# Kernel tuning notes

Measured on AMD Instinct MI355X. Metric: run time of the kernel, lower is better.

Reference implementation:

```python
import jax, jax.numpy as jnp
import numpy as np

D = 256
H = 4
HD = D // H


def rotate_half(x):
    xp = x.reshape(x.shape[:-1] + (-1, 2))
    x1, x2 = xp[..., 0], xp[..., 1]
    return jnp.stack((-x2, x1), axis=-1).reshape(x.shape)


def apply_rope(freqs, t):
    # freqs: [2, B, 1, N, HD]; t: [B, H, N, HD]
    return t * freqs[0] + rotate_half(t) * freqs[1]


def layernorm(x, g, b, eps=1e-5):
    m = jnp.mean(x, axis=-1, keepdims=True)
    v = jnp.var(x, axis=-1, keepdims=True)
    return (x - m) * jax.lax.rsqrt(v + eps) * g + b


def ffn(z, W1, b1, g, be, W2, b2):
    h = layernorm(z @ W1 + b1, g, be)
    h = jax.nn.gelu(h, approximate=False)
    return h @ W2 + b2


def heads_split(t):
    B, N, _ = t.shape
    return t.reshape(B, N, H, HD).transpose(0, 2, 1, 3)  # [B,H,N,HD]


def heads_merge(t):
    B, h, N, hd = t.shape
    return t.transpose(0, 2, 1, 3).reshape(B, N, h * hd)


def sdpa(q, k, v):
    s = q.shape[-1] ** (-0.5)
    sim = jnp.einsum('bhid,bhjd->bhij', q, k) * s
    attn = jax.nn.softmax(sim, axis=-1)
    return jnp.einsum('bhij,bhjd->bhid', attn, v)


def self_block(x, enc, Wqkv, bqkv, Wo, bo, W1, b1, g, be, W2, b2):
    B, N, _ = x.shape
    qkv = (x @ Wqkv + bqkv).reshape(B, N, H, HD, 3).transpose(0, 2, 1, 3, 4)
    q, k, v = qkv[..., 0], qkv[..., 1], qkv[..., 2]
    q = apply_rope(enc, q)
    k = apply_rope(enc, k)
    msg = heads_merge(sdpa(q, k, v)) @ Wo + bo
    return x + ffn(jnp.concatenate([x, msg], axis=-1), W1, b1, g, be, W2, b2)


def cross_block(x0, x1, Wqk, bqk, Wv, bv, Wo, bo, W1, b1, g, be, W2, b2):
    qk0 = heads_split(x0 @ Wqk + bqk)
    qk1 = heads_split(x1 @ Wqk + bqk)
    v0 = heads_split(x0 @ Wv + bv)
    v1 = heads_split(x1 @ Wv + bv)
    s = HD ** (-0.5)
    qk0 = qk0 * (s ** 0.5)
    qk1 = qk1 * (s ** 0.5)
    sim = jnp.einsum('bhid,bhjd->bhij', qk0, qk1)
    attn01 = jax.nn.softmax(sim, axis=-1)
    attn10 = jax.nn.softmax(sim.transpose(0, 1, 3, 2), axis=-1)
    m0 = jnp.einsum('bhij,bhjd->bhid', attn01, v1)
    m1 = jnp.einsum('bhij,bhjd->bhid', attn10, v0)
    m0 = heads_merge(m0) @ Wo + bo
    m1 = heads_merge(m1) @ Wo + bo
    x0 = x0 + ffn(jnp.concatenate([x0, m0], axis=-1), W1, b1, g, be, W2, b2)
    x1 = x1 + ffn(jnp.concatenate([x1, m1], axis=-1), W1, b1, g, be, W2, b2)
    return x0, x1


def setup_inputs() -> dict:
    key = jax.random.key(0)
    ks = jax.random.split(key, 24)
    B, N = 4, 2048
    desc0 = jax.random.normal(ks[0], (B, N, D), jnp.float32)
    desc1 = jax.random.normal(ks[1], (B, N, D), jnp.float32)
    encoding0 = jax.random.uniform(ks[2], (2, B, 1, N, HD), jnp.float32)
    encoding1 = jax.random.uniform(ks[3], (2, B, 1, N, HD), jnp.float32)

    def lin(k, fin, fout):
        k1, k2 = jax.random.split(k)
        W = jax.random.normal(k1, (fin, fout), jnp.float32) * (fin ** -0.5)
        b = jax.random.normal(k2, (fout,), jnp.float32) * 0.01
        return W, b

    Wqkv, bqkv = lin(ks[4], D, 3 * D)
    Wo_s, bo_s = lin(ks[5], D, D)
    W1_s, b1_s = lin(ks[6], 2 * D, 2 * D)
    g_s = jnp.ones((2 * D,), jnp.float32)
    be_s = jnp.zeros((2 * D,), jnp.float32)
    W2_s, b2_s = lin(ks[7], 2 * D, D)
    Wqk_c, bqk_c = lin(ks[8], D, D)
    Wv_c, bv_c = lin(ks[9], D, D)
    Wo_c, bo_c = lin(ks[10], D, D)
    W1_c, b1_c = lin(ks[11], 2 * D, 2 * D)
    g_c = jnp.ones((2 * D,), jnp.float32)
    be_c = jnp.zeros((2 * D,), jnp.float32)
    W2_c, b2_c = lin(ks[12], 2 * D, D)
    return dict(desc0=desc0, desc1=desc1, encoding0=encoding0, encoding1=encoding1,
                Wqkv=Wqkv, bqkv=bqkv, Wo_s=Wo_s, bo_s=bo_s,
                W1_s=W1_s, b1_s=b1_s, g_s=g_s, be_s=be_s, W2_s=W2_s, b2_s=b2_s,
                Wqk_c=Wqk_c, bqk_c=bqk_c, Wv_c=Wv_c, bv_c=bv_c, Wo_c=Wo_c, bo_c=bo_c,
                W1_c=W1_c, b1_c=b1_c, g_c=g_c, be_c=be_c, W2_c=W2_c, b2_c=b2_c)


def reference(desc0, desc1, encoding0, encoding1,
              Wqkv, bqkv, Wo_s, bo_s, W1_s, b1_s, g_s, be_s, W2_s, b2_s,
              Wqk_c, bqk_c, Wv_c, bv_c, Wo_c, bo_c, W1_c, b1_c, g_c, be_c, W2_c, b2_c):
    d0 = self_block(desc0, encoding0, Wqkv, bqkv, Wo_s, bo_s, W1_s, b1_s, g_s, be_s, W2_s, b2_s)
    d1 = self_block(desc1, encoding1, Wqkv, bqkv, Wo_s, bo_s, W1_s, b1_s, g_s, be_s, W2_s, b2_s)
    return cross_block(d0, d1, Wqk_c, bqk_c, Wv_c, bv_c, Wo_c, bo_c, W1_c, b1_c, g_c, be_c, W2_c, b2_c)
```

## Files before the change

kernel.cpp:

```cpp
#include <hip/hip_runtime.h>
#include <math.h>

#define BB 4
#define HH 4
#define NN 2048
#define DD 256
#define HDIM 64
#define NTOK 8192
#define NTOK2 16384

typedef __attribute__((ext_vector_type(8))) __bf16 bf16x8;
typedef __attribute__((ext_vector_type(8))) unsigned short ushort8;
typedef __attribute__((ext_vector_type(4))) float floatx4;
typedef __attribute__((ext_vector_type(4))) short short4v;

union U8 { ushort8 u; bf16x8 b; };
union U4 { unsigned int u[2]; unsigned long long l; short4v s; };

#define MFMA16(a, b, c) __builtin_amdgcn_mfma_f32_16x16x16bf16_1k(a, b, c, 0, 0, 0)

__device__ __forceinline__ unsigned short f2bf(float x) {
    unsigned int u = __float_as_uint(x);
    u += 0x7FFF + ((u >> 16) & 1);
    return (unsigned short)(u >> 16);
}
__device__ __forceinline__ float bf2f(unsigned short u) {
    return __uint_as_float(((unsigned int)u) << 16);
}
__device__ __forceinline__ unsigned int pkbf(float a, float b) {
    return ((__float_as_uint(a) + 0x8000u) >> 16) |
           ((__float_as_uint(b) + 0x8000u) & 0xFFFF0000u);
}

struct WTab {
    const float* w[9];
    unsigned short* o[9];
    int K[9];
    int N[9];
    int t0[10];
};

__global__ __launch_bounds__(256) void wtrans(WTab tab)
{
    __shared__ float lds[32][33];
    const int t = threadIdx.x;
    int bid = blockIdx.x;
    int s = 0;
    while (bid >= tab.t0[s + 1]) s++;
    const int ti = bid - tab.t0[s];
    const int K = tab.K[s], N = tab.N[s];
    const int tx = ti % (N / 32), ty = ti / (N / 32);
    const int k0 = ty * 32, n0 = tx * 32;
    const float* W = tab.w[s];
    unsigned short* Wt = tab.o[s];

    {
        int r = t >> 3, c = (t & 7) * 4;
        float4 a = *(const float4*)&W[(size_t)(k0 + r) * N + n0 + c];
        lds[r][c] = a.x; lds[r][c+1] = a.y; lds[r][c+2] = a.z; lds[r][c+3] = a.w;
    }
    __syncthreads();
    {
        int n = t >> 3, kq = (t & 7) * 4;
        ushort4 p;
        p.x = f2bf(lds[kq+0][n]); p.y = f2bf(lds[kq+1][n]);
        p.z = f2bf(lds[kq+2][n]); p.w = f2bf(lds[kq+3][n]);
        *(ushort4*)&Wt[(size_t)(n0 + n) * K + k0 + kq] = p;
    }
}

__global__ __launch_bounds__(256) void gemm_mfma(
    const unsigned short* __restrict__ A, int lda,
    const unsigned short* __restrict__ Wt, int K,
    const float* __restrict__ bias, const float* __restrict__ bias2, int mode,
    float* outF, unsigned short* outH0, unsigned short* outH1,
    unsigned short* outH2,
    int ldc, const float* R0, const float* R1)
{
    __shared__ __align__(16) unsigned short As[128 * 40];
    __shared__ __align__(16) unsigned short Bs[128 * 40];
    const int t = threadIdx.x;
    const int w = t >> 6, lane = t & 63, quad = lane >> 4, l15 = lane & 15;
    const int m0 = blockIdx.y * 128, n0 = blockIdx.x * 128;
    const int wm = (w >> 1) * 64, wn = (w & 1) * 64;
    const int sr = t >> 1, sc = (t & 1) * 16;

    const unsigned short* Ap = A  + (size_t)(m0 + sr) * lda + sc;
    const unsigned short* Bp = Wt + (size_t)(n0 + sr) * K   + sc;

    ushort8 pa0 = *(const ushort8*)(Ap);
    ushort8 pa1 = *(const ushort8*)(Ap + 8);
    ushort8 pb0 = *(const ushort8*)(Bp);
    ushort8 pb1 = *(const ushort8*)(Bp + 8);

    floatx4 acc[4][4];
    #pragma unroll
    for (int i = 0; i < 4; i++)
        #pragma unroll
        for (int j = 0; j < 4; j++) acc[i][j] = (floatx4){0.f, 0.f, 0.f, 0.f};

    const int nk = K >> 5;
    for (int kk = 0; kk < nk; kk++) {
        *(ushort8*)&As[sr * 40 + sc]     = pa0;
        *(ushort8*)&As[sr * 40 + sc + 8] = pa1;
        *(ushort8*)&Bs[sr * 40 + sc]     = pb0;
        *(ushort8*)&Bs[sr * 40 + sc + 8] = pb1;
        __syncthreads();
        if (kk + 1 < nk) {
            int ko = (kk + 1) * 32;
            pa0 = *(const ushort8*)(Ap + ko);
            pa1 = *(const ushort8*)(Ap + ko + 8);
            pb0 = *(const ushort8*)(Bp + ko);
            pb1 = *(const ushort8*)(Bp + ko + 8);
        }
        U8 af[4], bf[4];
        #pragma unroll
        for (int i = 0; i < 4; i++)
            af[i].u = *(const ushort8*)&As[(wm + i * 16 + l15) * 40 + quad * 8];
        #pragma unroll
        for (int j = 0; j < 4; j++)
            bf[j].u = *(const ushort8*)&Bs[(wn + j * 16 + l15) * 40 + quad * 8];
        #pragma unroll
        for (int i = 0; i < 4; i++)
            #pragma unroll
            for (int j = 0; j < 4; j++)
                acc[i][j] = __builtin_amdgcn_mfma_f32_16x16x32_bf16(af[i].b, bf[j].b, acc[i][j], 0, 0, 0);
        __syncthreads();
    }

    #pragma unroll
    for (int i = 0; i < 4; i++) {
        #pragma unroll
        for (int j = 0; j < 4; j++) {
            int col = n0 + wn + j * 16 + l15;
            float bv = (mode == 2 && col >= 256) ? bias2[col & 255] : bias[col];
            #pragma unroll
            for (int r = 0; r < 4; r++) {
                int grow = m0 + wm + i * 16 + quad * 4 + r;
                float v = acc[i][j][r] + bv;
                if (mode == 1) {
                    outH0[(size_t)grow * ldc + col] = f2bf(v);
                } else if (mode == 2) {
                    int cc = col & 255;
                    int h = cc >> 6, d = cc & 63;
                    int ds = grow >> 13, b = (grow >> 11) & 3, n = grow & 2047;
                    int bh = ds * 16 + b * 4 + h;
                    if (col < 256)
                        outH0[((size_t)bh * NN + n) * HDIM + d] = f2bf(v);
                    else
                        outH1[((size_t)bh * HDIM + d) * NN + n] = f2bf(v);
                } else if (mode == 3) {
                    int sel = col % 3, cc = col / 3;
                    int h = cc >> 6, d = cc & 63;
                    int ds = grow >> 13, b = (grow >> 11) & 3, n = grow & 2047;
                    int bh = ds * 16 + b * 4 + h;
                    if (sel == 0)
                        outH0[((size_t)bh * NN + n) * HDIM + d] = f2bf(v);
                    else if (sel == 1)
                        outH1[((size_t)bh * NN + n) * HDIM + d] = f2bf(v);
                    else
                        outH2[((size_t)bh * HDIM + d) * NN + n] = f2bf(v);
                } else {
                    const float* R = (grow < NTOK) ? R0 : R1;
                    float vv = v + R[(size_t)(grow & 8191) * 256 + col];
                    outF[(size_t)grow * 256 + col] = vv;
                    if (outH0) outH0[(size_t)grow * 256 + col] = f2bf(vv);
                    if (outH1) outH1[(size_t)grow * 512 + col] = f2bf(vv);
                }
            }
        }
    }
}

__global__ __launch_bounds__(256) void rope_k(unsigned short* __restrict__ qb,
                                              unsigned short* __restrict__ kb,
                                              const float* __restrict__ enc0,
                                              const float* __restrict__ enc1)
{
    int i = blockIdx.x * 256 + threadIdx.x;
    int dp = (i & 31) * 2;
    int n  = (i >> 5) & (NN - 1);
    int h  = (i >> 16) & 3;
    int b  = (i >> 18) & 3;
    int ds = (i >> 20) & 1;
    int bf = (i >> 21) & 1;
    unsigned short* tq = (bf ? kb : qb) +
        (((size_t)(ds * 16 + b * 4 + h)) * NN + n) * HDIM + dp;
    const float* e0 = (ds ? enc1 : enc0) + ((size_t)b * NN + n) * HDIM + dp;
    const float* e1 = e0 + (size_t)BB * NN * HDIM;
    float x0 = bf2f(tq[0]), x1 = bf2f(tq[1]);
    float y0 = x0 * e0[0] - x1 * e1[0];
    float y1 = x1 * e0[1] + x0 * e1[1];
    tq[0] = f2bf(y0); tq[1] = f2bf(y1);
}

__global__ __launch_bounds__(256) void flash_attn(
    const unsigned short* __restrict__ Q, const unsigned short* __restrict__ K,
    const unsigned short* __restrict__ V, unsigned short* __restrict__ O,
    int kvx, float qscale)
{
    __shared__ __align__(16) unsigned short Ks[64 * 72];
    __shared__ __align__(16) unsigned short Vt[64 * 72];

    const int t    = threadIdx.x;
    const int w    = t >> 6;
    const int lane = t & 63;
    const int quad = lane >> 4;
    const int l15  = lane & 15;
    const int bh   = blockIdx.y;
    const int kbh  = bh ^ kvx;
    const int q0   = blockIdx.x * 64;

    const unsigned short* Qb  = Q + (size_t)bh  * NN * HDIM;
    const unsigned short* Kb  = K + (size_t)kbh * NN * HDIM;
    const unsigned short* VTb = V + (size_t)kbh * NN * HDIM;

    const int srf = t >> 3, scf = (t & 7) * 8;

    const int qrow = q0 + w * 16 + l15;
    bf16x8 qf0, qf1;
    {
        U8 r0, r1, x0, x1;
        r0.u = *(const ushort8*)&Qb[(size_t)qrow * HDIM + quad * 8];
        r1.u = *(const ushort8*)&Qb[(size_t)qrow * HDIM + 32 + quad * 8];
        #pragma unroll
        for (int j = 0; j < 8; j++) {
            x0.u[j] = f2bf(bf2f(r0.u[j]) * qscale);
            x1.u[j] = f2bf(bf2f(r1.u[j]) * qscale);
        }
        qf0 = x0.b; qf1 = x1.b;
    }

    floatx4 o[4];
    #pragma unroll
    for (int c = 0; c < 4; c++) o[c] = (floatx4){0.f, 0.f, 0.f, 0.f};
    float m = -1e30f, l = 0.f;

    ushort8 ka0 = *(const ushort8*)&Kb[(size_t)srf * HDIM + scf];
    ushort8 ka1 = *(const ushort8*)&Kb[(size_t)(srf + 32) * HDIM + scf];
    ushort8 va0 = *(const ushort8*)&VTb[(size_t)srf * NN + scf];
    ushort8 va1 = *(const ushort8*)&VTb[(size_t)(srf + 32) * NN + scf];

    for (int j0 = 0; j0 < NN; j0 += 64) {
        *(ushort8*)&Ks[srf * 72 + scf]        = ka0;
        *(ushort8*)&Ks[(srf + 32) * 72 + scf] = ka1;
        *(ushort8*)&Vt[srf * 72 + scf]        = va0;
        *(ushort8*)&Vt[(srf + 32) * 72 + scf] = va1;
        __syncthreads();
        if (j0 + 64 < NN) {
            int jn = j0 + 64;
            ka0 = *(const ushort8*)&Kb[(size_t)(jn + srf) * HDIM + scf];
            ka1 = *(const ushort8*)&Kb[(size_t)(jn + srf + 32) * HDIM + scf];
            va0 = *(const ushort8*)&VTb[(size_t)srf * NN + jn + scf];
            va1 = *(const ushort8*)&VTb[(size_t)(srf + 32) * NN + jn + scf];
        }

        floatx4 s[4];
        #pragma unroll
        for (int t4 = 0; t4 < 4; t4++) {
            U8 k0, k1;
            k0.u = *(const ushort8*)&Ks[(t4 * 16 + l15) * 72 + quad * 8];
            k1.u = *(const ushort8*)&Ks[(t4 * 16 + l15) * 72 + 32 + quad * 8];
            floatx4 z = (floatx4){0.f, 0.f, 0.f, 0.f};
            z = __builtin_amdgcn_mfma_f32_16x16x32_bf16(k0.b, qf0, z, 0, 0, 0);
            z = __builtin_amdgcn_mfma_f32_16x16x32_bf16(k1.b, qf1, z, 0, 0, 0);
            s[t4] = z;
        }

        float mx = s[0][0];
        #pragma unroll
        for (int t4 = 0; t4 < 4; t4++)
            #pragma unroll
            for (int r = 0; r < 4; r++) mx = fmaxf(mx, s[t4][r]);
        mx = fmaxf(mx, __shfl_xor(mx, 16, 64));
        mx = fmaxf(mx, __shfl_xor(mx, 32, 64));
        float mn = fmaxf(m, mx);
        float al = exp2f(m - mn);
        m = mn;
        float rs = 0.f;
        #pragma unroll
        for (int t4 = 0; t4 < 4; t4++)
            #pragma unroll
            for (int r = 0; r < 4; r++) {
                float p = exp2f(s[t4][r] - mn);
                s[t4][r] = p;
                rs += p;
            }
        rs += __shfl_xor(rs, 16, 64);
        rs += __shfl_xor(rs, 32, 64);
        l = l * al + rs;
        #pragma unroll
        for (int c = 0; c < 4; c++)
            #pragma unroll
            for (int r = 0; r < 4; r++) o[c][r] *= al;

        short4v pf[4];
        #pragma unroll
        for (int t4 = 0; t4 < 4; t4++) {
            U4 pk;
            pk.u[0] = pkbf(s[t4][0], s[t4][1]);
            pk.u[1] = pkbf(s[t4][2], s[t4][3]);
            pf[t4] = pk.s;
        }

        #pragma unroll
        for (int c = 0; c < 4; c++) {
            #pragma unroll
            for (int t4 = 0; t4 < 4; t4++) {
                U4 vf;
                vf.l = *(const unsigned long long*)
                    &Vt[(c * 16 + l15) * 72 + t4 * 16 + quad * 4];
                o[c] = MFMA16(vf.s, pf[t4], o[c]);
            }
        }
        __syncthreads();
    }

    const int ds = bh >> 4, b = (bh >> 2) & 3, h = bh & 3;
    const int q = q0 + w * 16 + l15;
    const size_t row = (size_t)ds * NTOK + b * NN + q;
    float inv = 1.f / l;
    #pragma unroll
    for (int c = 0; c < 4; c++) {
        ushort4 pk;
        pk.x = f2bf(o[c][0] * inv);
        pk.y = f2bf(o[c][1] * inv);
        pk.z = f2bf(o[c][2] * inv);
        pk.w = f2bf(o[c][3] * inv);
        *(ushort4*)&O[row * DD + h * HDIM + c * 16 + quad * 4] = pk;
    }
}

__global__ __launch_bounds__(256) void ln_gelu(
    unsigned short* __restrict__ hb, const float* __restrict__ g,
    const float* __restrict__ be)
{
    __shared__ float r1[4], r2[4];
    const int t = threadIdx.x;
    const size_t row = blockIdx.x;
    unsigned short* ip = hb + row * 512;
    float x0 = bf2f(ip[t]), x1 = bf2f(ip[t + 256]);
    float s = x0 + x1, ss = x0 * x0 + x1 * x1;
    #pragma unroll
    for (int o = 32; o > 0; o >>= 1) { s += __shfl_down(s, o); ss += __shfl_down(ss, o); }
    if ((t & 63) == 0) { r1[t >> 6] = s; r2[t >> 6] = ss; }
    __syncthreads();
    float S  = r1[0] + r1[1] + r1[2] + r1[3];
    float SS = r2[0] + r2[1] + r2[2] + r2[3];
    float mean = S * (1.f / 512.f);
    float var  = SS * (1.f / 512.f) - mean * mean;
    float inv  = rsqrtf(var + 1e-5f);
    float y0 = (x0 - mean) * inv * g[t]       + be[t];
    float y1 = (x1 - mean) * inv * g[t + 256] + be[t + 256];
    ip[t]       = f2bf(0.5f * y0 * (1.f + erff(y0 * 0.70710678f)));
    ip[t + 256] = f2bf(0.5f * y1 * (1.f + erff(y1 * 0.70710678f)));
}

__global__ __launch_bounds__(256) void copy_to_cat(
    const float* __restrict__ s0, const float* __restrict__ s1,
    unsigned short* __restrict__ cat)
{
    int i = blockIdx.x * 256 + threadIdx.x;
    int row = i >> 6, c4 = (i & 63) * 4;
    const float* s = (row < NTOK) ? s0 : s1;
    float4 a = *(const float4*)&s[(size_t)(row & 8191) * 256 + c4];
    ushort4 p = { f2bf(a.x), f2bf(a.y), f2bf(a.z), f2bf(a.w) };
    *(ushort4*)&cat[(size_t)row * 512 + c4] = p;
}

extern "C" void kernel_launch(void* const* d_in, const int* in_sizes, int n_in,
                              void* d_out, int out_size, void* d_ws, size_t ws_size,
                              hipStream_t stream)
{
    const float* desc0 = (const float*)d_in[0];
    const float* desc1 = (const float*)d_in[1];
    const float* enc0  = (const float*)d_in[2];
    const float* enc1  = (const float*)d_in[3];
    const float* Wqkv  = (const float*)d_in[4];  const float* bqkv  = (const float*)d_in[5];
    const float* Wo_s  = (const float*)d_in[6];  const float* bo_s  = (const float*)d_in[7];
    const float* W1_s  = (const float*)d_in[8];  const float* b1_s  = (const float*)d_in[9];
    const float* g_s   = (const float*)d_in[10]; const float* be_s  = (const float*)d_in[11];
    const float* W2_s  = (const float*)d_in[12]; const float* b2_s  = (const float*)d_in[13];
    const float* Wqk_c = (const float*)d_in[14]; const float* bqk_c = (const float*)d_in[15];
    const float* Wv_c  = (const float*)d_in[16]; const float* bv_c  = (const float*)d_in[17];
    const float* Wo_c  = (const float*)d_in[18]; const float* bo_c  = (const float*)d_in[19];
    const float* W1_c  = (const float*)d_in[20]; const float* b1_c  = (const float*)d_in[21];
    const float* g_c   = (const float*)d_in[22]; const float* be_c  = (const float*)d_in[23];
    const float* W2_c  = (const float*)d_in[24]; const float* b2_c  = (const float*)d_in[25];

    char* ws = (char*)d_ws;
    unsigned short* wt  = (unsigned short*)ws;
    unsigned short* qb  = (unsigned short*)(ws + 2490368);
    unsigned short* kb  = (unsigned short*)(ws + 10878976);
    unsigned short* msg = (unsigned short*)(ws + 19267584);
    unsigned short* vb  = (unsigned short*)(ws + 27656192);
    unsigned short* cat = (unsigned short*)(ws + 36044800);
    unsigned short* hb  = (unsigned short*)(ws + 52822016);
    unsigned short* dbf = (unsigned short*)(ws + 86376448);

    unsigned short* t_qkv = wt;
    unsigned short* t_wos = wt + 196608;
    unsigned short* t_w1s = wt + 262144;
    unsigned short* t_w2s = wt + 524288;
    unsigned short* t_wqk = wt + 655360;
    unsigned short* t_wv  = wt + 720896;
    unsigned short* t_woc = wt + 786432;
    unsigned short* t_w1c = wt + 851968;
    unsigned short* t_w2c = wt + 1114112;

    float* outF = (float*)d_out;

    dim3 blk(256);

    WTab tab;
    tab.w[0] = Wqkv;  tab.o[0] = t_qkv; tab.K[0] = 256; tab.N[0] = 768;
    tab.w[1] = Wo_s;  tab.o[1] = t_wos; tab.K[1] = 256; tab.N[1] = 256;
    tab.w[2] = W1_s;  tab.o[2] = t_w1s; tab.K[2] = 512; tab.N[2] = 512;
    tab.w[3] = W2_s;  tab.o[3] = t_w2s; tab.K[3] = 512; tab.N[3] = 256;
    tab.w[4] = Wqk_c; tab.o[4] = t_wqk; tab.K[4] = 256; tab.N[4] = 256;
    tab.w[5] = Wv_c;  tab.o[5] = t_wv;  tab.K[5] = 256; tab.N[5] = 256;
    tab.w[6] = Wo_c;  tab.o[6] = t_woc; tab.K[6] = 256; tab.N[6] = 256;
    tab.w[7] = W1_c;  tab.o[7] = t_w1c; tab.K[7] = 512; tab.N[7] = 512;
    tab.w[8] = W2_c;  tab.o[8] = t_w2c; tab.K[8] = 512; tab.N[8] = 256;
    int acc_t = 0;
    for (int s = 0; s < 9; s++) {
        tab.t0[s] = acc_t;
        acc_t += (tab.K[s] / 32) * (tab.N[s] / 32);
    }
    tab.t0[9] = acc_t;
    hipLaunchKernelGGL(wtrans, dim3(acc_t), blk, 0, stream, tab);

    auto gemm = [&](const unsigned short* A, int lda, const unsigned short* Wtp,
                    int K, const float* bias, const float* bias2, int Nc, int mode,
                    float* oF, unsigned short* oh0, unsigned short* oh1,
                    unsigned short* oh2, int ldc, const float* r0, const float* r1) {
        dim3 g(Nc / 128, NTOK2 / 128);
        hipLaunchKernelGGL(gemm_mfma, g, blk, 0, stream,
                           A, lda, Wtp, K, bias, bias2, mode,
                           oF, oh0, oh1, oh2, ldc, r0, r1);
    };

    const float QS = 0.125f * 1.44269504088896f;

    hipLaunchKernelGGL(copy_to_cat, dim3(4096), blk, 0, stream, desc0, desc1, cat);
    gemm(cat, 512, t_qkv, 256, bqkv, nullptr, 768, 3,
         nullptr, qb, kb, vb, 0, nullptr, nullptr);
    hipLaunchKernelGGL(rope_k, dim3(16384), blk, 0, stream, qb, kb, enc0, enc1);
    hipLaunchKernelGGL(flash_attn, dim3(NN / 64, 32), blk, 0, stream,
                       qb, kb, vb, msg, 0, QS);
    gemm(msg, 256, t_wos, 256, bo_s, nullptr, 256, 1,
         nullptr, cat + 256, nullptr, nullptr, 512, nullptr, nullptr);
    gemm(cat, 512, t_w1s, 512, b1_s, nullptr, 512, 1,
         nullptr, hb, nullptr, nullptr, 512, nullptr, nullptr);
    hipLaunchKernelGGL(ln_gelu, dim3(NTOK2), blk, 0, stream, hb, g_s, be_s);
    gemm(hb, 512, t_w2s, 512, b2_s, nullptr, 256, 4,
         outF, dbf, cat, nullptr, 256, desc0, desc1);

    gemm(dbf, 256, t_wqk, 256, bqk_c, bv_c, 512, 2,
         nullptr, qb, vb, nullptr, 0, nullptr, nullptr);
    hipLaunchKernelGGL(flash_attn, dim3(NN / 64, 32), blk, 0, stream,
                       qb, qb, vb, msg, 16, QS);
    gemm(msg, 256, t_woc, 256, bo_c, nullptr, 256, 1,
         nullptr, cat + 256, nullptr, nullptr, 512, nullptr, nullptr);
    gemm(cat, 512, t_w1c, 512, b1_c, nullptr, 512, 1,
         nullptr, hb, nullptr, nullptr, 512, nullptr, nullptr);
    hipLaunchKernelGGL(ln_gelu, dim3(NTOK2), blk, 0, stream, hb, g_c, be_c);
    gemm(hb, 512, t_w2c, 512, b2_c, nullptr, 256, 4,
         outF, nullptr, nullptr, nullptr, 256, outF, outF + (size_t)NTOK * 256);
}
```

Baseline: 533.3 us.

## Fold output projection into FFN first layer and shrink GEMM tile to 64x128

Precomputes Wo·W1[256:] and bo·W1[256:]+b1 once per call for both the self and cross blocks. The attention output can then be written straight into the concat buffer, which removes two full Wo GEMMs and the msg buffer round trip. It also changes the GEMM tiling from 128x128 to 64x128 per block, doubling the grid. The risks are extra bf16 rounding from the fused weights and less reuse per block.

New measurement: 494.2 us. -7.3%, faster.

```diff
diff --git a/kernel.cpp b/kernel.cpp
--- a/kernel.cpp
+++ b/kernel.cpp
@@ -33,11 +33,12 @@
 }
 
 struct WTab {
-    const float* w[9];
-    unsigned short* o[9];
-    int K[9];
-    int N[9];
-    int t0[10];
+    const float* w[7];
+    unsigned short* o[7];
+    int K[7];
+    int N[7];
+    int st[7];
+    int t0[8];
 };
 
 __global__ __launch_bounds__(256) void wtrans(WTab tab)
@@ -48,7 +49,7 @@
     int s = 0;
     while (bid >= tab.t0[s + 1]) s++;
     const int ti = bid - tab.t0[s];
-    const int K = tab.K[s], N = tab.N[s];
+    const int K = tab.K[s], N = tab.N[s], st = tab.st[s];
     const int tx = ti % (N / 32), ty = ti / (N / 32);
     const int k0 = ty * 32, n0 = tx * 32;
     const float* W = tab.w[s];
@@ -65,8 +66,63 @@
         ushort4 p;
         p.x = f2bf(lds[kq+0][n]); p.y = f2bf(lds[kq+1][n]);
         p.z = f2bf(lds[kq+2][n]); p.w = f2bf(lds[kq+3][n]);
-        *(ushort4*)&Wt[(size_t)(n0 + n) * K + k0 + kq] = p;
-    }
+        *(ushort4*)&Wt[(size_t)(n0 + n) * st + k0 + kq] = p;
+    }
+}
+
+__global__ __launch_bounds__(256) void wfuse(
+    const float* __restrict__ Wo_s, const float* __restrict__ W1_s,
+    unsigned short* __restrict__ o_s,
+    const float* __restrict__ Wo_c, const float* __restrict__ W1_c,
+    unsigned short* __restrict__ o_c)
+{
+    __shared__ float wo[32][33];
+    __shared__ float w1[32][68];
+    const int t = threadIdx.x;
+    const int bid = blockIdx.x;
+    const int seg = bid >> 6, ti_ = bid & 63;
+    const int i0 = (ti_ >> 3) * 32, n0 = (ti_ & 7) * 64;
+    const float* Wo  = seg ? Wo_c : Wo_s;
+    const float* W1b = (seg ? W1_c : W1_s) + 256 * 512;
+    unsigned short* out = seg ? o_c : o_s;
+    const int ti = t >> 3, tn = t & 7;
+
+    float acc[8] = {};
+    for (int jc = 0; jc < 256; jc += 32) {
+        {
+            int r = t >> 3, c = (t & 7) * 4;
+            *(float4*)&wo[r][c] = *(const float4*)&Wo[(size_t)(i0 + r) * 256 + jc + c];
+            int c8 = (t & 7) * 8;
+            *(float4*)&w1[r][c8]     = *(const float4*)&W1b[(size_t)(jc + r) * 512 + n0 + c8];
+            *(float4*)&w1[r][c8 + 4] = *(const float4*)&W1b[(size_t)(jc + r) * 512 + n0 + c8 + 4];
+        }
+        __syncthreads();
+        #pragma unroll
+        for (int j = 0; j < 32; j++) {
+            float a = wo[ti][j];
+            #pragma unroll
+            for (int e = 0; e < 8; e++) acc[e] += a * w1[j][tn * 8 + e];
+        }
+        __syncthreads();
+    }
+    #pragma unroll
+    for (int e = 0; e < 8; e++)
+        out[(size_t)(n0 + tn * 8 + e) * 512 + 256 + i0 + ti] = f2bf(acc[e]);
+}
+
+__global__ __launch_bounds__(256) void bfuse(
+    const float* bo_s, const float* W1_s, const float* b1_s, float* bs,
+    const float* bo_c, const float* W1_c, const float* b1_c, float* bc)
+{
+    const int seg = blockIdx.x >> 1, half = blockIdx.x & 1;
+    const int n = half * 256 + threadIdx.x;
+    const float* bo  = seg ? bo_c : bo_s;
+    const float* W1b = (seg ? W1_c : W1_s) + 256 * 512;
+    const float* b1  = seg ? b1_c : b1_s;
+    float* out       = seg ? bc : bs;
+    float a = b1[n];
+    for (int j = 0; j < 256; j++) a += bo[j] * W1b[(size_t)j * 512 + n];
+    out[n] = a;
 }
 
 __global__ __launch_bounds__(256) void gemm_mfma(
@@ -77,53 +133,51 @@
     unsigned short* outH2,
     int ldc, const float* R0, const float* R1)
 {
-    __shared__ __align__(16) unsigned short As[128 * 40];
+    __shared__ __align__(16) unsigned short As[64 * 40];
     __shared__ __align__(16) unsigned short Bs[128 * 40];
     const int t = threadIdx.x;
     const int w = t >> 6, lane = t & 63, quad = lane >> 4, l15 = lane & 15;
-    const int m0 = blockIdx.y * 128, n0 = blockIdx.x * 128;
-    const int wm = (w >> 1) * 64, wn = (w & 1) * 64;
-    const int sr = t >> 1, sc = (t & 1) * 16;
-
-    const unsigned short* Ap = A  + (size_t)(m0 + sr) * lda + sc;
-    const unsigned short* Bp = Wt + (size_t)(n0 + sr) * K   + sc;
-
-    ushort8 pa0 = *(const ushort8*)(Ap);
-    ushort8 pa1 = *(const ushort8*)(Ap + 8);
+    const int m0 = blockIdx.y * 64, n0 = blockIdx.x * 128;
+    const int wn = w * 32;
+    const int sar = t >> 2, sac = (t & 3) * 8;
+    const int sbr = t >> 1, sbc = (t & 1) * 16;
+
+    const unsigned short* Ap = A  + (size_t)(m0 + sar) * lda + sac;
+    const unsigned short* Bp = Wt + (size_t)(n0 + sbr) * K   + sbc;
+
+    ushort8 pa  = *(const ushort8*)(Ap);
     ushort8 pb0 = *(const ushort8*)(Bp);
     ushort8 pb1 = *(const ushort8*)(Bp + 8);
 
-    floatx4 acc[4][4];
+    floatx4 acc[4][2];
     #pragma unroll
     for (int i = 0; i < 4; i++)
         #pragma unroll
-        for (int j = 0; j < 4; j++) acc[i][j] = (floatx4){0.f, 0.f, 0.f, 0.f};
+        for (int j = 0; j < 2; j++) acc[i][j] = (floatx4){0.f, 0.f, 0.f, 0.f};
 
     const int nk = K >> 5;
     for (int kk = 0; kk < nk; kk++) {
-        *(ushort8*)&As[sr * 40 + sc]     = pa0;
-        *(ushort8*)&As[sr * 40 + sc + 8] = pa1;
-        *(ushort8*)&Bs[sr * 40 + sc]     = pb0;
-        *(ushort8*)&Bs[sr * 40 + sc + 8] = pb1;
+        *(ushort8*)&As[sar * 40 + sac]     = pa;
+        *(ushort8*)&Bs[sbr * 40 + sbc]     = pb0;
+        *(ushort8*)&Bs[sbr * 40 + sbc + 8] = pb1;
         __syncthreads();
         if (kk + 1 < nk) {
             int ko = (kk + 1) * 32;
-            pa0 = *(const ushort8*)(Ap + ko);
-            pa1 = *(const ushort8*)(Ap + ko + 8);
+            pa  = *(const ushort8*)(Ap + ko);
             pb0 = *(const ushort8*)(Bp + ko);
             pb1 = *(const ushort8*)(Bp + ko + 8);
         }
-        U8 af[4], bf[4];
+        U8 af[4], bf[2];
         #pragma unroll
         for (int i = 0; i < 4; i++)
-            af[i].u = *(const ushort8*)&As[(wm + i * 16 + l15) * 40 + quad * 8];
-        #pragma unroll
-        for (int j = 0; j < 4; j++)
+            af[i].u = *(const ushort8*)&As[(i * 16 + l15) * 40 + quad * 8];
+        #pragma unroll
+        for (int j = 0; j < 2; j++)
             bf[j].u = *(const ushort8*)&Bs[(wn + j * 16 + l15) * 40 + quad * 8];
         #pragma unroll
         for (int i = 0; i < 4; i++)
             #pragma unroll
-            for (int j = 0; j < 4; j++)
+            for (int j = 0; j < 2; j++)
                 acc[i][j] = __builtin_amdgcn_mfma_f32_16x16x32_bf16(af[i].b, bf[j].b, acc[i][j], 0, 0, 0);
         __syncthreads();
     }
@@ -131,12 +185,12 @@
     #pragma unroll
     for (int i = 0; i < 4; i++) {
         #pragma unroll
-        for (int j = 0; j < 4; j++) {
+        for (int j = 0; j < 2; j++) {
             int col = n0 + wn + j * 16 + l15;
             float bv = (mode == 2 && col >= 256) ? bias2[col & 255] : bias[col];
             #pragma unroll
             for (int r = 0; r < 4; r++) {
-                int grow = m0 + wm + i * 16 + quad * 4 + r;
+                int grow = m0 + i * 16 + quad * 4 + r;
                 float v = acc[i][j][r] + bv;
                 if (mode == 1) {
                     outH0[(size_t)grow * ldc + col] = f2bf(v);
@@ -197,7 +251,7 @@
 __global__ __launch_bounds__(256) void flash_attn(
     const unsigned short* __restrict__ Q, const unsigned short* __restrict__ K,
     const unsigned short* __restrict__ V, unsigned short* __restrict__ O,
-    int kvx, float qscale)
+    int ldo, int kvx, float qscale)
 {
     __shared__ __align__(16) unsigned short Ks[64 * 72];
     __shared__ __align__(16) unsigned short Vt[64 * 72];
@@ -327,7 +381,7 @@
         pk.y = f2bf(o[c][1] * inv);
         pk.z = f2bf(o[c][2] * inv);
         pk.w = f2bf(o[c][3] * inv);
-        *(ushort4*)&O[row * DD + h * HDIM + c * 16 + quad * 4] = pk;
+        *(ushort4*)&O[row * ldo + h * HDIM + c * 16 + quad * 4] = pk;
     }
 }
 
@@ -392,49 +446,49 @@
     unsigned short* wt  = (unsigned short*)ws;
     unsigned short* qb  = (unsigned short*)(ws + 2490368);
     unsigned short* kb  = (unsigned short*)(ws + 10878976);
-    unsigned short* msg = (unsigned short*)(ws + 19267584);
     unsigned short* vb  = (unsigned short*)(ws + 27656192);
     unsigned short* cat = (unsigned short*)(ws + 36044800);
     unsigned short* hb  = (unsigned short*)(ws + 52822016);
     unsigned short* dbf = (unsigned short*)(ws + 86376448);
 
-    unsigned short* t_qkv = wt;
-    unsigned short* t_wos = wt + 196608;
-    unsigned short* t_w1s = wt + 262144;
-    unsigned short* t_w2s = wt + 524288;
-    unsigned short* t_wqk = wt + 655360;
-    unsigned short* t_wv  = wt + 720896;
-    unsigned short* t_woc = wt + 786432;
-    unsigned short* t_w1c = wt + 851968;
-    unsigned short* t_w2c = wt + 1114112;
+    unsigned short* t_qkv  = wt;
+    float*          bias_s = (float*)(wt + 196608);
+    unsigned short* t_w1s  = wt + 262144;
+    unsigned short* t_w2s  = wt + 524288;
+    unsigned short* t_wqkc = wt + 655360;
+    float*          bias_c = (float*)(wt + 786432);
+    unsigned short* t_w1c  = wt + 851968;
+    unsigned short* t_w2c  = wt + 1114112;
 
     float* outF = (float*)d_out;
 
     dim3 blk(256);
 
     WTab tab;
-    tab.w[0] = Wqkv;  tab.o[0] = t_qkv; tab.K[0] = 256; tab.N[0] = 768;
-    tab.w[1] = Wo_s;  tab.o[1] = t_wos; tab.K[1] = 256; tab.N[1] = 256;
-    tab.w[2] = W1_s;  tab.o[2] = t_w1s; tab.K[2] = 512; tab.N[2] = 512;
-    tab.w[3] = W2_s;  tab.o[3] = t_w2s; tab.K[3] = 512; tab.N[3] = 256;
-    tab.w[4] = Wqk_c; tab.o[4] = t_wqk; tab.K[4] = 256; tab.N[4] = 256;
-    tab.w[5] = Wv_c;  tab.o[5] = t_wv;  tab.K[5] = 256; tab.N[5] = 256;
-    tab.w[6] = Wo_c;  tab.o[6] = t_woc; tab.K[6] = 256; tab.N[6] = 256;
-    tab.w[7] = W1_c;  tab.o[7] = t_w1c; tab.K[7] = 512; tab.N[7] = 512;
-    tab.w[8] = W2_c;  tab.o[8] = t_w2c; tab.K[8] = 512; tab.N[8] = 256;
+    tab.w[0] = Wqkv;  tab.o[0] = t_qkv;          tab.K[0] = 256; tab.N[0] = 768; tab.st[0] = 256;
+    tab.w[1] = W1_s;  tab.o[1] = t_w1s;          tab.K[1] = 256; tab.N[1] = 512; tab.st[1] = 512;
+    tab.w[2] = W2_s;  tab.o[2] = t_w2s;          tab.K[2] = 512; tab.N[2] = 256; tab.st[2] = 512;
+    tab.w[3] = Wqk_c; tab.o[3] = t_wqkc;         tab.K[3] = 256; tab.N[3] = 256; tab.st[3] = 256;
+    tab.w[4] = Wv_c;  tab.o[4] = t_wqkc + 65536; tab.K[4] = 256; tab.N[4] = 256; tab.st[4] = 256;
+    tab.w[5] = W1_c;  tab.o[5] = t_w1c;          tab.K[5] = 256; tab.N[5] = 512; tab.st[5] = 512;
+    tab.w[6] = W2_c;  tab.o[6] = t_w2c;          tab.K[6] = 512; tab.N[6] = 256; tab.st[6] = 512;
     int acc_t = 0;
-    for (int s = 0; s < 9; s++) {
+    for (int s = 0; s < 7; s++) {
         tab.t0[s] = acc_t;
         acc_t += (tab.K[s] / 32) * (tab.N[s] / 32);
     }
-    tab.t0[9] = acc_t;
+    tab.t0[7] = acc_t;
     hipLaunchKernelGGL(wtrans, dim3(acc_t), blk, 0, stream, tab);
+    hipLaunchKernelGGL(wfuse, dim3(128), blk, 0, stream,
+                       Wo_s, W1_s, t_w1s, Wo_c, W1_c, t_w1c);
+    hipLaunchKernelGGL(bfuse, dim3(4), blk, 0, stream,
+                       bo_s, W1_s, b1_s, bias_s, bo_c, W1_c, b1_c, bias_c);
 
     auto gemm = [&](const unsigned short* A, int lda, const unsigned short* Wtp,
                     int K, const float* bias, const float* bias2, int Nc, int mode,
                     float* oF, unsigned short* oh0, unsigned short* oh1,
                     unsigned short* oh2, int ldc, const float* r0, const float* r1) {
-        dim3 g(Nc / 128, NTOK2 / 128);
+        dim3 g(Nc / 128, NTOK2 / 64);
         hipLaunchKernelGGL(gemm_mfma, g, blk, 0, stream,
                            A, lda, Wtp, K, bias, bias2, mode,
                            oF, oh0, oh1, oh2, ldc, r0, r1);
@@ -447,22 +501,18 @@
          nullptr, qb, kb, vb, 0, nullptr, nullptr);
     hipLaunchKernelGGL(rope_k, dim3(16384), blk, 0, stream, qb, kb, enc0, enc1);
     hipLaunchKernelGGL(flash_attn, dim3(NN / 64, 32), blk, 0, stream,
-                       qb, kb, vb, msg, 0, QS);
-    gemm(msg, 256, t_wos, 256, bo_s, nullptr, 256, 1,
-         nullptr, cat + 256, nullptr, nullptr, 512, nullptr, nullptr);
-    gemm(cat, 512, t_w1s, 512, b1_s, nullptr, 512, 1,
+                       qb, kb, vb, cat + 256, 512, 0, QS);
+    gemm(cat, 512, t_w1s, 512, bias_s, nullptr, 512, 1,
          nullptr, hb, nullptr, nullptr, 512, nullptr, nullptr);
     hipLaunchKernelGGL(ln_gelu, dim3(NTOK2), blk, 0, stream, hb, g_s, be_s);
     gemm(hb, 512, t_w2s, 512, b2_s, nullptr, 256, 4,
          outF, dbf, cat, nullptr, 256, desc0, desc1);
 
-    gemm(dbf, 256, t_wqk, 256, bqk_c, bv_c, 512, 2,
+    gemm(dbf, 256, t_wqkc, 256, bqk_c, bv_c, 512, 2,
          nullptr, qb, vb, nullptr, 0, nullptr, nullptr);
     hipLaunchKernelGGL(flash_attn, dim3(NN / 64, 32), blk, 0, stream,
-                       qb, qb, vb, msg, 16, QS);
-    gemm(msg, 256, t_woc, 256, bo_c, nullptr, 256, 1,
-         nullptr, cat + 256, nullptr, nullptr, 512, nullptr, nullptr);
-    gemm(cat, 512, t_w1c, 512, b1_c, nullptr, 512, 1,
+                       qb, qb, vb, cat + 256, 512, 16, QS);
+    gemm(cat, 512, t_w1c, 512, bias_c, nullptr, 512, 1,
          nullptr, hb, nullptr, nullptr, 512, nullptr, nullptr);
     hipLaunchKernelGGL(ln_gelu, dim3(NTOK2), blk, 0, stream, hb, g_c, be_c);
     gemm(hb, 512, t_w2c, 512, b2_c, nullptr, 256, 4,
```
